# Kernel optimization log

Measured on AMD Instinct MI355X. Metric: run time of the kernel, lower is better.

## Reference

```python
import jax, jax.numpy as jnp
import numpy as np

D_MODEL = 1024
NUM_HEADS = 16
HEAD_DIM = D_MODEL // NUM_HEADS
B, TQ, TK = 4, 2048, 2048


def setup_inputs() -> dict:
    key = jax.random.key(0)
    ks = jax.random.split(key, 6)
    s = 1.0 / np.sqrt(D_MODEL)
    return {
        "x_q": jax.random.normal(ks[0], (B, TQ, D_MODEL), dtype=jnp.float32),
        "x_kv": jax.random.normal(ks[1], (B, TK, D_MODEL), dtype=jnp.float32),
        "attn_mask": jnp.zeros((TQ, TK), dtype=jnp.float32),
        "key_padding_mask": jnp.zeros((B, TK), dtype=bool),
        "Wq": jax.random.normal(ks[2], (D_MODEL, D_MODEL), dtype=jnp.float32) * s,
        "Wk": jax.random.normal(ks[3], (D_MODEL, D_MODEL), dtype=jnp.float32) * s,
        "Wv": jax.random.normal(ks[4], (D_MODEL, D_MODEL), dtype=jnp.float32) * s,
        "Wo": jax.random.normal(ks[5], (D_MODEL, D_MODEL), dtype=jnp.float32) * s,
    }


def reference(x_q, x_kv, attn_mask, key_padding_mask, Wq, Wk, Wv, Wo):
    b, tq, d = x_q.shape
    tk = x_kv.shape[1]
    h, hd = NUM_HEADS, HEAD_DIM
    # Linear(bias=False): y = x @ W.T ; split heads -> (b, h, t, hd)
    q = (x_q @ Wq.T).reshape(b, tq, h, hd).transpose(0, 2, 1, 3)
    k = (x_kv @ Wk.T).reshape(b, tk, h, hd).transpose(0, 2, 1, 3)
    v = (x_kv @ Wv.T).reshape(b, tk, h, hd).transpose(0, 2, 1, 3)
    scores = jnp.einsum("bhqd,bhkd->bhqk", q, k) / jnp.sqrt(jnp.float32(hd))
    scores = scores + attn_mask  # additive mask broadcasts over (b, h)
    scores = jnp.where(key_padding_mask[:, None, None, :], -jnp.inf, scores)
    w = jax.nn.softmax(scores, axis=-1)
    out = jnp.einsum("bhqk,bhkd->bhqd", w, v)  # (b, h, tq, hd)
    out = out.transpose(0, 2, 1, 3).reshape(b, tq, d)
    return out @ Wo.T
```

## Files before the change

### kernel.cpp

```cpp
#include <hip/hip_runtime.h>
#include <hip/hip_bf16.h>

#define TQ 2048
#define TKV 2048
#define NH 16
#define HD 64
#define DM 1024
#define BSZ 4
#define LOG2E 1.44269504088896340736f

typedef __bf16 bf16_t;
typedef bf16_t bf16x8 __attribute__((ext_vector_type(8)));
typedef bf16_t bf16x4 __attribute__((ext_vector_type(4)));
typedef float f32x4 __attribute__((ext_vector_type(4)));

__device__ __forceinline__ f32x4 MFMA16(bf16x8 a, bf16x8 b, f32x4 c) {
  return __builtin_amdgcn_mfma_f32_16x16x32_bf16(a, b, c, 0, 0, 0);
}

__device__ __forceinline__ void gload_lds16(const void* g, void* l) {
  __builtin_amdgcn_global_load_lds((const __attribute__((address_space(1))) void*)g,
                                   (__attribute__((address_space(3))) void*)l,
                                   16, 0, 0);
}

__device__ __forceinline__ int pl_idx(int q, int k) {
  int bb = (k >> 3) ^ (q & 7);
  return q * 64 + bb * 8 + (k & 7);
}

__device__ __forceinline__ int kv_idx(int row, int slot) {
  return row * 64 + (slot ^ (row & 7)) * 8;
}

__global__ __launch_bounds__(256) void cvt_all(
    const float* __restrict__ xq, const float* __restrict__ xkv,
    const float* __restrict__ wq, const float* __restrict__ wk,
    const float* __restrict__ wv, const float* __restrict__ wo,
    const unsigned char* __restrict__ kpad,
    bf16_t* __restrict__ oxq, bf16_t* __restrict__ oxkv,
    bf16_t* __restrict__ owq, bf16_t* __restrict__ owk,
    bf16_t* __restrict__ owv, bf16_t* __restrict__ owo,
    bf16_t* __restrict__ okpd) {
  const int blk = blockIdx.x;
  if (blk >= 10240) {
    const int i = (blk - 10240) * 256 + threadIdx.x;
    unsigned long long bits = *reinterpret_cast<const unsigned long long*>(kpad + (size_t)i * 8);
    bf16x8 o;
#pragma unroll
    for (int j = 0; j < 8; ++j)
      o[j] = ((bits >> (8 * j)) & 0xffull) ? (bf16_t)(-__builtin_inff()) : (bf16_t)0.f;
    reinterpret_cast<bf16x8*>(okpd)[i] = o;
    return;
  }
  const float* src;
  bf16_t* dst;
  int base;
  if (blk < 4096)      { src = xq;  dst = oxq;  base = blk; }
  else if (blk < 8192) { src = xkv; dst = oxkv; base = blk - 4096; }
  else if (blk < 8704) { src = wq;  dst = owq;  base = blk - 8192; }
  else if (blk < 9216) { src = wk;  dst = owk;  base = blk - 8704; }
  else if (blk < 9728) { src = wv;  dst = owv;  base = blk - 9216; }
  else                 { src = wo;  dst = owo;  base = blk - 9728; }
  const int i = base * 256 + threadIdx.x;
  const float4* p = reinterpret_cast<const float4*>(src) + 2 * (size_t)i;
  float4 a = p[0], b = p[1];
  bf16x8 o;
  o[0] = (bf16_t)a.x; o[1] = (bf16_t)a.y; o[2] = (bf16_t)a.z; o[3] = (bf16_t)a.w;
  o[4] = (bf16_t)b.x; o[5] = (bf16_t)b.y; o[6] = (bf16_t)b.z; o[7] = (bf16_t)b.w;
  reinterpret_cast<bf16x8*>(dst)[i] = o;
}

__global__ __launch_bounds__(256) void tmask(const float* __restrict__ am,
                                             bf16_t* __restrict__ amt) {
  __shared__ float T[64][65];
  const int q0 = blockIdx.x * 64, k0 = blockIdx.y * 64;
  const int tid = threadIdx.x;
  const int r = tid >> 2, c4 = (tid & 3) * 4;
#pragma unroll
  for (int cc = 0; cc < 4; ++cc) {
    const int kc = c4 + cc * 16;
    float4 v = *reinterpret_cast<const float4*>(am + (long)(q0 + r) * TKV + k0 + kc);
    T[kc + 0][r] = v.x; T[kc + 1][r] = v.y; T[kc + 2][r] = v.z; T[kc + 3][r] = v.w;
  }
  __syncthreads();
  const int kr = tid >> 2, qc0 = (tid & 3) * 16;
  bf16x8 o0, o1;
#pragma unroll
  for (int j = 0; j < 8; ++j) o0[j] = (bf16_t)(T[kr][qc0 + j] * LOG2E);
#pragma unroll
  for (int j = 0; j < 8; ++j) o1[j] = (bf16_t)(T[kr][qc0 + 8 + j] * LOG2E);
  *reinterpret_cast<bf16x8*>(amt + (long)(k0 + kr) * TQ + q0 + qc0) = o0;
  *reinterpret_cast<bf16x8*>(amt + (long)(k0 + kr) * TQ + q0 + qc0 + 8) = o1;
}

template <bool BF16_OUT>
__global__ __launch_bounds__(256) void gemm_bt(const bf16_t* __restrict__ A,
                                               const bf16_t* __restrict__ Bw,
                                               void* __restrict__ Cout,
                                               int M, int N, int K, float scale) {
  __shared__ __align__(16) bf16_t As[128 * 32];
  __shared__ __align__(16) bf16_t Bs[128 * 32];
  const int tid = threadIdx.x;
  const int l = tid & 63;
  const int w = tid >> 6;
  const int wr = w >> 1, wc = w & 1;
  const int l15 = l & 15, lg = l >> 4;
  const long bm = (long)blockIdx.x * 128;
  const long bn = (long)blockIdx.y * 128;

  f32x4 acc[4][4] = {};
  const int c0i = tid, c1i = 256 + tid;
  const long ar0 = (bm + (c0i >> 2)) * (long)K + (c0i & 3) * 8;
  const long ar1 = (bm + (c1i >> 2)) * (long)K + (c1i & 3) * 8;
  const long br0 = (bn + (c0i >> 2)) * (long)K + (c0i & 3) * 8;
  const long br1 = (bn + (c1i >> 2)) * (long)K + (c1i & 3) * 8;

  for (int k0 = 0; k0 < K; k0 += 32) {
    __syncthreads();
    gload_lds16(A + ar0 + k0, As + c0i * 8);
    gload_lds16(A + ar1 + k0, As + c1i * 8);
    gload_lds16(Bw + br0 + k0, Bs + c0i * 8);
    gload_lds16(Bw + br1 + k0, Bs + c1i * 8);
    __syncthreads();

    bf16x8 af[4], bfr[4];
#pragma unroll
    for (int i = 0; i < 4; ++i)
      af[i] = *reinterpret_cast<const bf16x8*>(As + (wr * 64 + i * 16 + l15) * 32 + lg * 8);
#pragma unroll
    for (int j = 0; j < 4; ++j)
      bfr[j] = *reinterpret_cast<const bf16x8*>(Bs + (wc * 64 + j * 16 + l15) * 32 + lg * 8);
#pragma unroll
    for (int i = 0; i < 4; ++i)
#pragma unroll
      for (int j = 0; j < 4; ++j)
        acc[i][j] = MFMA16(af[i], bfr[j], acc[i][j]);
  }

#pragma unroll
  for (int i = 0; i < 4; ++i)
#pragma unroll
    for (int j = 0; j < 4; ++j)
#pragma unroll
      for (int r = 0; r < 4; ++r) {
        long rg = bm + wr * 64 + i * 16 + lg * 4 + r;
        long cg = bn + wc * 64 + j * 16 + l15;
        float v = acc[i][j][r] * scale;
        if (BF16_OUT) ((bf16_t*)Cout)[rg * N + cg] = (bf16_t)v;
        else          ((float*)Cout)[rg * N + cg] = v;
      }
}

__global__ __launch_bounds__(256) void gemm_kv(const bf16_t* __restrict__ A,
                                               const bf16_t* __restrict__ Bw,
                                               bf16_t* __restrict__ Kb,
                                               bf16_t* __restrict__ VTb) {
  __shared__ __align__(16) bf16_t As[128 * 32];
  __shared__ __align__(16) bf16_t Bs[128 * 32];
  const int K = DM;
  const int tid = threadIdx.x;
  const int l = tid & 63;
  const int w = tid >> 6;
  const int wr = w >> 1, wc = w & 1;
  const int l15 = l & 15, lg = l >> 4;
  const long bm = (long)blockIdx.x * 128;
  const long bn = (long)blockIdx.y * 128;

  f32x4 acc[4][4] = {};
  const int c0i = tid, c1i = 256 + tid;
  const long ar0 = (bm + (c0i >> 2)) * (long)K + (c0i & 3) * 8;
  const long ar1 = (bm + (c1i >> 2)) * (long)K + (c1i & 3) * 8;
  const long br0 = (bn + (c0i >> 2)) * (long)K + (c0i & 3) * 8;
  const long br1 = (bn + (c1i >> 2)) * (long)K + (c1i & 3) * 8;

  for (int k0 = 0; k0 < K; k0 += 32) {
    __syncthreads();
    gload_lds16(A + ar0 + k0, As + c0i * 8);
    gload_lds16(A + ar1 + k0, As + c1i * 8);
    gload_lds16(Bw + br0 + k0, Bs + c0i * 8);
    gload_lds16(Bw + br1 + k0, Bs + c1i * 8);
    __syncthreads();

    bf16x8 af[4], bfr[4];
#pragma unroll
    for (int i = 0; i < 4; ++i)
      af[i] = *reinterpret_cast<const bf16x8*>(As + (wr * 64 + i * 16 + l15) * 32 + lg * 8);
#pragma unroll
    for (int j = 0; j < 4; ++j)
      bfr[j] = *reinterpret_cast<const bf16x8*>(Bs + (wc * 64 + j * 16 + l15) * 32 + lg * 8);
#pragma unroll
    for (int i = 0; i < 4; ++i)
#pragma unroll
      for (int j = 0; j < 4; ++j)
        acc[i][j] = MFMA16(af[i], bfr[j], acc[i][j]);
  }

  if (bn < 1024) {
#pragma unroll
    for (int i = 0; i < 4; ++i)
#pragma unroll
      for (int j = 0; j < 4; ++j)
#pragma unroll
        for (int r = 0; r < 4; ++r) {
          long rg = bm + wr * 64 + i * 16 + lg * 4 + r;
          long cg = bn + wc * 64 + j * 16 + l15;
          Kb[rg * DM + cg] = (bf16_t)acc[i][j][r];
        }
  } else {
    const long brow = (bm >> 11) * (long)DM;
    const long t0 = (bm & 2047);
#pragma unroll
    for (int i = 0; i < 4; ++i)
#pragma unroll
      for (int j = 0; j < 4; ++j) {
        long d = bn - 1024 + wc * 64 + j * 16 + l15;
        long t = t0 + wr * 64 + i * 16 + lg * 4;
        bf16x4 pk;
#pragma unroll
        for (int r = 0; r < 4; ++r) pk[r] = (bf16_t)acc[i][j][r];
        *reinterpret_cast<bf16x4*>(VTb + (brow + d) * TKV + t) = pk;
      }
  }
}

__global__ __launch_bounds__(256) void attn_fwd(const bf16_t* __restrict__ Qb,
                                                const bf16_t* __restrict__ Kb,
                                                const bf16_t* __restrict__ VTb,
                                                const bf16_t* __restrict__ amt,
                                                const bf16_t* __restrict__ kpd,
                                                bf16_t* __restrict__ Ob) {
  __shared__ __align__(16) bf16_t Ks[2][64 * 64];
  __shared__ __align__(16) bf16_t Vs[2][64 * 64];
  __shared__ __align__(16) bf16_t Pl[4][16 * 64];
  const int tid = threadIdx.x;
  const int w = tid >> 6, l = tid & 63;
  const int l15 = l & 15, lg = l >> 4;
  const int b = blockIdx.y >> 4, h = blockIdx.y & 15;
  const int q0 = blockIdx.x * 64 + w * 16;
  const long qbase = (long)b * TQ * DM;

  const bf16_t* qp = Qb + qbase + (long)(q0 + l15) * DM + h * HD + lg * 8;
  bf16x8 qf0 = *reinterpret_cast<const bf16x8*>(qp);
  bf16x8 qf1 = *reinterpret_cast<const bf16x8*>(qp + 32);

  const bf16_t* kg = Kb + qbase + h * HD;
  const bf16_t* vtg = VTb + ((long)b * DM + h * HD) * (long)TKV;

  const int srow0 = tid >> 3, spos0 = tid & 7;
  const int soff0 = (spos0 ^ (srow0 & 7)) * 8;
  const int srow1 = (tid + 256) >> 3, spos1 = tid & 7;
  const int soff1 = (spos1 ^ (srow1 & 7)) * 8;

  f32x4 o[4] = {};
  float m[4], ls[4];
#pragma unroll
  for (int r = 0; r < 4; ++r) { m[r] = -1e30f; ls[r] = 0.f; }

  gload_lds16(kg + (long)srow0 * DM + soff0, &Ks[0][tid * 8]);
  gload_lds16(kg + (long)srow1 * DM + soff1, &Ks[0][(tid + 256) * 8]);
  gload_lds16(vtg + (long)srow0 * TKV + soff0, &Vs[0][tid * 8]);
  gload_lds16(vtg + (long)srow1 * TKV + soff1, &Vs[0][(tid + 256) * 8]);
  __syncthreads();

  int cur = 0;
  const int NT = TKV / 64;
  for (int t = 0; t < NT; ++t) {
    const int k0 = t * 64;
    if (t + 1 < NT) {
      const long kn = (long)(k0 + 64);
      gload_lds16(kg + (kn + srow0) * DM + soff0, &Ks[cur ^ 1][tid * 8]);
      gload_lds16(kg + (kn + srow1) * DM + soff1, &Ks[cur ^ 1][(tid + 256) * 8]);
      gload_lds16(vtg + (long)srow0 * TKV + kn + soff0, &Vs[cur ^ 1][tid * 8]);
      gload_lds16(vtg + (long)srow1 * TKV + kn + soff1, &Vs[cur ^ 1][(tid + 256) * 8]);
    }
    const bf16_t* Kc = Ks[cur];
    const bf16_t* Vc = Vs[cur];

    bf16x4 mt[4];
    float kpf[4];
#pragma unroll
    for (int f = 0; f < 4; ++f) {
      mt[f] = *reinterpret_cast<const bf16x4*>(amt + (long)(k0 + 16 * f + l15) * TQ + q0 + lg * 4);
      kpf[f] = (float)kpd[b * TKV + k0 + 16 * f + l15];
    }

    f32x4 c[4] = {};
#pragma unroll
    for (int f = 0; f < 4; ++f) {
      const int row = 16 * f + l15;
      bf16x8 ka = *reinterpret_cast<const bf16x8*>(Kc + kv_idx(row, lg));
      bf16x8 kb = *reinterpret_cast<const bf16x8*>(Kc + kv_idx(row, 4 + lg));
      c[f] = MFMA16(qf0, ka, c[f]);
      c[f] = MFMA16(qf1, kb, c[f]);
    }

#pragma unroll
    for (int r = 0; r < 4; ++r) {
      float s0 = c[0][r] + (float)mt[0][r] + kpf[0];
      float s1 = c[1][r] + (float)mt[1][r] + kpf[1];
      float s2 = c[2][r] + (float)mt[2][r] + kpf[2];
      float s3 = c[3][r] + (float)mt[3][r] + kpf[3];
      float rmax = fmaxf(fmaxf(s0, s1), fmaxf(s2, s3));
#pragma unroll
      for (int d = 1; d < 16; d <<= 1) rmax = fmaxf(rmax, __shfl_xor(rmax, d, 64));
      const float mn = fmaxf(m[r], rmax);
      const float fac = exp2f(m[r] - mn);
      m[r] = mn;
      const float p0 = exp2f(s0 - mn);
      const float p1 = exp2f(s1 - mn);
      const float p2 = exp2f(s2 - mn);
      const float p3 = exp2f(s3 - mn);
      ls[r] = ls[r] * fac + (p0 + p1 + p2 + p3);
      o[0][r] *= fac; o[1][r] *= fac; o[2][r] *= fac; o[3][r] *= fac;
      const int q = lg * 4 + r;
      Pl[w][pl_idx(q, l15)]      = (bf16_t)p0;
      Pl[w][pl_idx(q, 16 + l15)] = (bf16_t)p1;
      Pl[w][pl_idx(q, 32 + l15)] = (bf16_t)p2;
      Pl[w][pl_idx(q, 48 + l15)] = (bf16_t)p3;
    }

#pragma unroll
    for (int hh = 0; hh < 2; ++hh) {
      bf16x8 pf = *reinterpret_cast<const bf16x8*>(&Pl[w][pl_idx(l15, hh * 32 + lg * 8)]);
#pragma unroll
      for (int f = 0; f < 4; ++f) {
        const int row = 16 * f + l15;
        bf16x8 vf = *reinterpret_cast<const bf16x8*>(Vc + kv_idx(row, hh * 4 + lg));
        o[f] = MFMA16(pf, vf, o[f]);
      }
    }

    __syncthreads();
    cur ^= 1;
  }

#pragma unroll
  for (int r = 0; r < 4; ++r) {
    float t = ls[r];
#pragma unroll
    for (int d = 1; d < 16; d <<= 1) t += __shfl_xor(t, d, 64);
    const float inv = t > 0.f ? 1.f / t : 0.f;
    const long qg = q0 + lg * 4 + r;
    bf16_t* op = Ob + qbase + qg * DM + h * HD;
    op[l15]      = (bf16_t)(o[0][r] * inv);
    op[16 + l15] = (bf16_t)(o[1][r] * inv);
    op[32 + l15] = (bf16_t)(o[2][r] * inv);
    op[48 + l15] = (bf16_t)(o[3][r] * inv);
  }
}

extern "C" void kernel_launch(void* const* d_in, const int* in_sizes, int n_in,
                              void* d_out, int out_size, void* d_ws, size_t ws_size,
                              hipStream_t stream) {
  const float* x_q = (const float*)d_in[0];
  const float* x_kv = (const float*)d_in[1];
  const float* amask = (const float*)d_in[2];
  const unsigned char* kpad = (const unsigned char*)d_in[3];
  const float* Wq = (const float*)d_in[4];
  const float* Wk = (const float*)d_in[5];
  const float* Wv = (const float*)d_in[6];
  const float* Wo = (const float*)d_in[7];
  float* out = (float*)d_out;

  char* ws = (char*)d_ws;
  const size_t MB = 1024ull * 1024ull;
  bf16_t* Ob    = (bf16_t*)(ws + 0 * MB);
  bf16_t* xq_b  = (bf16_t*)(ws + 0 * MB);
  bf16_t* xkv_b = (bf16_t*)(ws + 16 * MB);
  bf16_t* Qb    = (bf16_t*)(ws + 32 * MB);
  bf16_t* Kb    = (bf16_t*)(ws + 48 * MB);
  bf16_t* VTb   = (bf16_t*)(ws + 64 * MB);
  bf16_t* amt   = (bf16_t*)(ws + 80 * MB);
  bf16_t* Wq_b  = (bf16_t*)(ws + 88 * MB);
  bf16_t* Wk_b  = (bf16_t*)(ws + 90 * MB);
  bf16_t* Wv_b  = (bf16_t*)(ws + 92 * MB);
  bf16_t* Wo_b  = (bf16_t*)(ws + 94 * MB);
  bf16_t* kpdd  = (bf16_t*)(ws + 96 * MB);

  const int NTOK = BSZ * TQ;

  cvt_all<<<10244, 256, 0, stream>>>(x_q, x_kv, Wq, Wk, Wv, Wo, kpad,
                                     xq_b, xkv_b, Wq_b, Wk_b, Wv_b, Wo_b, kpdd);
  tmask<<<dim3(TQ / 64, TKV / 64), 256, 0, stream>>>(amask, amt);

  gemm_bt<true><<<dim3(NTOK / 128, DM / 128), 256, 0, stream>>>(
      xq_b, Wq_b, Qb, NTOK, DM, DM, 0.125f * LOG2E);
  gemm_kv<<<dim3(NTOK / 128, 2 * DM / 128), 256, 0, stream>>>(xkv_b, Wk_b, Kb, VTb);

  attn_fwd<<<dim3(TQ / 64, BSZ * NH), 256, 0, stream>>>(Qb, Kb, VTb, amt, kpdd, Ob);

  gemm_bt<false><<<dim3(NTOK / 128, DM / 128), 256, 0, stream>>>(
      Ob, Wo_b, out, NTOK, DM, DM, 1.f);
}
```

Baseline: 557.2 us.

## Fold padding mask into per-batch bias, double query rows per warp, lazy rescale

Attention blocks now handle 128 query rows, with each warp processing two 16-row groups. This reuses each K/V LDS fragment across two MFMA groups and halves K/V tile loads per query. The key padding mask is combined with the additive mask into a per-batch bf16 bias tensor, which preloads the score accumulator and removes the separate padding load. Online softmax now rescales only when the row max grows by more than 8 (log2 units). Blocks are also remapped for locality. The costs are a 4x larger mask tensor (32MB written and read), higher register pressure, and half as many blocks.

```diff
diff --git a/kernel.cpp b/kernel.cpp
--- a/kernel.cpp
+++ b/kernel.cpp
@@ -37,22 +37,10 @@
     const float* __restrict__ xq, const float* __restrict__ xkv,
     const float* __restrict__ wq, const float* __restrict__ wk,
     const float* __restrict__ wv, const float* __restrict__ wo,
-    const unsigned char* __restrict__ kpad,
     bf16_t* __restrict__ oxq, bf16_t* __restrict__ oxkv,
     bf16_t* __restrict__ owq, bf16_t* __restrict__ owk,
-    bf16_t* __restrict__ owv, bf16_t* __restrict__ owo,
-    bf16_t* __restrict__ okpd) {
+    bf16_t* __restrict__ owv, bf16_t* __restrict__ owo) {
   const int blk = blockIdx.x;
-  if (blk >= 10240) {
-    const int i = (blk - 10240) * 256 + threadIdx.x;
-    unsigned long long bits = *reinterpret_cast<const unsigned long long*>(kpad + (size_t)i * 8);
-    bf16x8 o;
-#pragma unroll
-    for (int j = 0; j < 8; ++j)
-      o[j] = ((bits >> (8 * j)) & 0xffull) ? (bf16_t)(-__builtin_inff()) : (bf16_t)0.f;
-    reinterpret_cast<bf16x8*>(okpd)[i] = o;
-    return;
-  }
   const float* src;
   bf16_t* dst;
   int base;
@@ -71,8 +59,9 @@
   reinterpret_cast<bf16x8*>(dst)[i] = o;
 }
 
-__global__ __launch_bounds__(256) void tmask(const float* __restrict__ am,
-                                             bf16_t* __restrict__ amt) {
+__global__ __launch_bounds__(256) void tmask2(const float* __restrict__ am,
+                                              const unsigned char* __restrict__ kpad,
+                                              bf16_t* __restrict__ amt2) {
   __shared__ float T[64][65];
   const int q0 = blockIdx.x * 64, k0 = blockIdx.y * 64;
   const int tid = threadIdx.x;
@@ -85,13 +74,21 @@
   }
   __syncthreads();
   const int kr = tid >> 2, qc0 = (tid & 3) * 16;
-  bf16x8 o0, o1;
-#pragma unroll
-  for (int j = 0; j < 8; ++j) o0[j] = (bf16_t)(T[kr][qc0 + j] * LOG2E);
-#pragma unroll
-  for (int j = 0; j < 8; ++j) o1[j] = (bf16_t)(T[kr][qc0 + 8 + j] * LOG2E);
-  *reinterpret_cast<bf16x8*>(amt + (long)(k0 + kr) * TQ + q0 + qc0) = o0;
-  *reinterpret_cast<bf16x8*>(amt + (long)(k0 + kr) * TQ + q0 + qc0 + 8) = o1;
+  float mk[16];
+#pragma unroll
+  for (int j = 0; j < 16; ++j) mk[j] = T[kr][qc0 + j] * LOG2E;
+#pragma unroll
+  for (int b = 0; b < BSZ; ++b) {
+    const float kv = kpad[b * TKV + k0 + kr] ? -__builtin_inff() : 0.f;
+    bf16x8 o0, o1;
+#pragma unroll
+    for (int j = 0; j < 8; ++j) o0[j] = (bf16_t)(mk[j] + kv);
+#pragma unroll
+    for (int j = 0; j < 8; ++j) o1[j] = (bf16_t)(mk[8 + j] + kv);
+    bf16_t* dst = amt2 + ((long)b * TKV + k0 + kr) * TQ + q0 + qc0;
+    *reinterpret_cast<bf16x8*>(dst) = o0;
+    *reinterpret_cast<bf16x8*>(dst + 8) = o1;
+  }
 }
 
 template <bool BF16_OUT>
@@ -227,8 +224,7 @@
 __global__ __launch_bounds__(256) void attn_fwd(const bf16_t* __restrict__ Qb,
                                                 const bf16_t* __restrict__ Kb,
                                                 const bf16_t* __restrict__ VTb,
-                                                const bf16_t* __restrict__ amt,
-                                                const bf16_t* __restrict__ kpd,
+                                                const bf16_t* __restrict__ amt2,
                                                 bf16_t* __restrict__ Ob) {
   __shared__ __align__(16) bf16_t Ks[2][64 * 64];
   __shared__ __align__(16) bf16_t Vs[2][64 * 64];
@@ -236,26 +232,36 @@
   const int tid = threadIdx.x;
   const int w = tid >> 6, l = tid & 63;
   const int l15 = l & 15, lg = l >> 4;
-  const int b = blockIdx.y >> 4, h = blockIdx.y & 15;
-  const int q0 = blockIdx.x * 64 + w * 16;
+
+  const int flat = blockIdx.y * 16 + blockIdx.x;
+  const int nid = (flat & 7) * 128 + (flat >> 3);
+  const int bh = nid >> 4, qb = nid & 15;
+  const int b = bh >> 4, h = bh & 15;
+  const int q0 = qb * 128 + w * 32;
   const long qbase = (long)b * TQ * DM;
 
   const bf16_t* qp = Qb + qbase + (long)(q0 + l15) * DM + h * HD + lg * 8;
-  bf16x8 qf0 = *reinterpret_cast<const bf16x8*>(qp);
-  bf16x8 qf1 = *reinterpret_cast<const bf16x8*>(qp + 32);
+  bf16x8 qf[2][2];
+  qf[0][0] = *reinterpret_cast<const bf16x8*>(qp);
+  qf[0][1] = *reinterpret_cast<const bf16x8*>(qp + 32);
+  qf[1][0] = *reinterpret_cast<const bf16x8*>(qp + 16 * DM);
+  qf[1][1] = *reinterpret_cast<const bf16x8*>(qp + 16 * DM + 32);
 
   const bf16_t* kg = Kb + qbase + h * HD;
   const bf16_t* vtg = VTb + ((long)b * DM + h * HD) * (long)TKV;
-
-  const int srow0 = tid >> 3, spos0 = tid & 7;
-  const int soff0 = (spos0 ^ (srow0 & 7)) * 8;
-  const int srow1 = (tid + 256) >> 3, spos1 = tid & 7;
-  const int soff1 = (spos1 ^ (srow1 & 7)) * 8;
-
-  f32x4 o[4] = {};
-  float m[4], ls[4];
-#pragma unroll
-  for (int r = 0; r < 4; ++r) { m[r] = -1e30f; ls[r] = 0.f; }
+  const bf16_t* m2 = amt2 + (long)b * TKV * TQ;
+
+  const int srow0 = tid >> 3;
+  const int soff0 = ((tid & 7) ^ (srow0 & 7)) * 8;
+  const int srow1 = (tid + 256) >> 3;
+  const int soff1 = ((tid & 7) ^ (srow1 & 7)) * 8;
+
+  f32x4 o[2][4] = {};
+  float m[2][4], ls[2][4];
+#pragma unroll
+  for (int g = 0; g < 2; ++g)
+#pragma unroll
+    for (int r = 0; r < 4; ++r) { m[g][r] = -1e30f; ls[g][r] = 0.f; }
 
   gload_lds16(kg + (long)srow0 * DM + soff0, &Ks[0][tid * 8]);
   gload_lds16(kg + (long)srow1 * DM + soff1, &Ks[0][(tid + 256) * 8]);
@@ -277,77 +283,92 @@
     const bf16_t* Kc = Ks[cur];
     const bf16_t* Vc = Vs[cur];
 
-    bf16x4 mt[4];
-    float kpf[4];
-#pragma unroll
-    for (int f = 0; f < 4; ++f) {
-      mt[f] = *reinterpret_cast<const bf16x4*>(amt + (long)(k0 + 16 * f + l15) * TQ + q0 + lg * 4);
-      kpf[f] = (float)kpd[b * TKV + k0 + 16 * f + l15];
-    }
-
-    f32x4 c[4] = {};
+    bf16x4 mt[2][4];
+#pragma unroll
+    for (int g = 0; g < 2; ++g)
+#pragma unroll
+      for (int f = 0; f < 4; ++f)
+        mt[g][f] = *reinterpret_cast<const bf16x4*>(
+            m2 + (long)(k0 + 16 * f + l15) * TQ + q0 + g * 16 + lg * 4);
+
+    f32x4 c[2][4];
+#pragma unroll
+    for (int g = 0; g < 2; ++g)
+#pragma unroll
+      for (int f = 0; f < 4; ++f)
+#pragma unroll
+        for (int r = 0; r < 4; ++r) c[g][f][r] = (float)mt[g][f][r];
+
 #pragma unroll
     for (int f = 0; f < 4; ++f) {
       const int row = 16 * f + l15;
       bf16x8 ka = *reinterpret_cast<const bf16x8*>(Kc + kv_idx(row, lg));
-      bf16x8 kb = *reinterpret_cast<const bf16x8*>(Kc + kv_idx(row, 4 + lg));
-      c[f] = MFMA16(qf0, ka, c[f]);
-      c[f] = MFMA16(qf1, kb, c[f]);
-    }
-
-#pragma unroll
-    for (int r = 0; r < 4; ++r) {
-      float s0 = c[0][r] + (float)mt[0][r] + kpf[0];
-      float s1 = c[1][r] + (float)mt[1][r] + kpf[1];
-      float s2 = c[2][r] + (float)mt[2][r] + kpf[2];
-      float s3 = c[3][r] + (float)mt[3][r] + kpf[3];
-      float rmax = fmaxf(fmaxf(s0, s1), fmaxf(s2, s3));
-#pragma unroll
-      for (int d = 1; d < 16; d <<= 1) rmax = fmaxf(rmax, __shfl_xor(rmax, d, 64));
-      const float mn = fmaxf(m[r], rmax);
-      const float fac = exp2f(m[r] - mn);
-      m[r] = mn;
-      const float p0 = exp2f(s0 - mn);
-      const float p1 = exp2f(s1 - mn);
-      const float p2 = exp2f(s2 - mn);
-      const float p3 = exp2f(s3 - mn);
-      ls[r] = ls[r] * fac + (p0 + p1 + p2 + p3);
-      o[0][r] *= fac; o[1][r] *= fac; o[2][r] *= fac; o[3][r] *= fac;
-      const int q = lg * 4 + r;
-      Pl[w][pl_idx(q, l15)]      = (bf16_t)p0;
-      Pl[w][pl_idx(q, 16 + l15)] = (bf16_t)p1;
-      Pl[w][pl_idx(q, 32 + l15)] = (bf16_t)p2;
-      Pl[w][pl_idx(q, 48 + l15)] = (bf16_t)p3;
-    }
-
-#pragma unroll
-    for (int hh = 0; hh < 2; ++hh) {
-      bf16x8 pf = *reinterpret_cast<const bf16x8*>(&Pl[w][pl_idx(l15, hh * 32 + lg * 8)]);
-#pragma unroll
-      for (int f = 0; f < 4; ++f) {
-        const int row = 16 * f + l15;
-        bf16x8 vf = *reinterpret_cast<const bf16x8*>(Vc + kv_idx(row, hh * 4 + lg));
-        o[f] = MFMA16(pf, vf, o[f]);
+      bf16x8 kb2 = *reinterpret_cast<const bf16x8*>(Kc + kv_idx(row, 4 + lg));
+#pragma unroll
+      for (int g = 0; g < 2; ++g) {
+        c[g][f] = MFMA16(qf[g][0], ka, c[g][f]);
+        c[g][f] = MFMA16(qf[g][1], kb2, c[g][f]);
       }
     }
 
+#pragma unroll
+    for (int g = 0; g < 2; ++g) {
+#pragma unroll
+      for (int r = 0; r < 4; ++r) {
+        const float s0 = c[g][0][r], s1 = c[g][1][r];
+        const float s2 = c[g][2][r], s3 = c[g][3][r];
+        float rmax = fmaxf(fmaxf(s0, s1), fmaxf(s2, s3));
+#pragma unroll
+        for (int d = 1; d < 16; d <<= 1) rmax = fmaxf(rmax, __shfl_xor(rmax, d, 64));
+        if (!__all(rmax <= m[g][r] + 8.f)) {
+          const float mn = fmaxf(m[g][r], rmax);
+          const float fac = exp2f(m[g][r] - mn);
+          ls[g][r] *= fac;
+          o[g][0][r] *= fac; o[g][1][r] *= fac;
+          o[g][2][r] *= fac; o[g][3][r] *= fac;
+          m[g][r] = mn;
+        }
+        const float p0 = exp2f(s0 - m[g][r]);
+        const float p1 = exp2f(s1 - m[g][r]);
+        const float p2 = exp2f(s2 - m[g][r]);
+        const float p3 = exp2f(s3 - m[g][r]);
+        ls[g][r] += (p0 + p1) + (p2 + p3);
+        const int q = lg * 4 + r;
+        Pl[w][pl_idx(q, l15)]      = (bf16_t)p0;
+        Pl[w][pl_idx(q, 16 + l15)] = (bf16_t)p1;
+        Pl[w][pl_idx(q, 32 + l15)] = (bf16_t)p2;
+        Pl[w][pl_idx(q, 48 + l15)] = (bf16_t)p3;
+      }
+#pragma unroll
+      for (int hh = 0; hh < 2; ++hh) {
+        bf16x8 pf = *reinterpret_cast<const bf16x8*>(&Pl[w][pl_idx(l15, hh * 32 + lg * 8)]);
+#pragma unroll
+        for (int f = 0; f < 4; ++f) {
+          bf16x8 vf = *reinterpret_cast<const bf16x8*>(Vc + kv_idx(16 * f + l15, hh * 4 + lg));
+          o[g][f] = MFMA16(pf, vf, o[g][f]);
+        }
+      }
+    }
+
     __syncthreads();
     cur ^= 1;
   }
 
 #pragma unroll
-  for (int r = 0; r < 4; ++r) {
-    float t = ls[r];
-#pragma unroll
-    for (int d = 1; d < 16; d <<= 1) t += __shfl_xor(t, d, 64);
-    const float inv = t > 0.f ? 1.f / t : 0.f;
-    const long qg = q0 + lg * 4 + r;
-    bf16_t* op = Ob + qbase + qg * DM + h * HD;
-    op[l15]      = (bf16_t)(o[0][r] * inv);
-    op[16 + l15] = (bf16_t)(o[1][r] * inv);
-    op[32 + l15] = (bf16_t)(o[2][r] * inv);
-    op[48 + l15] = (bf16_t)(o[3][r] * inv);
-  }
+  for (int g = 0; g < 2; ++g)
+#pragma unroll
+    for (int r = 0; r < 4; ++r) {
+      float t = ls[g][r];
+#pragma unroll
+      for (int d = 1; d < 16; d <<= 1) t += __shfl_xor(t, d, 64);
+      const float inv = t > 0.f ? 1.f / t : 0.f;
+      const long qg = q0 + g * 16 + lg * 4 + r;
+      bf16_t* op = Ob + qbase + qg * DM + h * HD;
+      op[l15]      = (bf16_t)(o[g][0][r] * inv);
+      op[16 + l15] = (bf16_t)(o[g][1][r] * inv);
+      op[32 + l15] = (bf16_t)(o[g][2][r] * inv);
+      op[48 + l15] = (bf16_t)(o[g][3][r] * inv);
+    }
 }
 
 extern "C" void kernel_launch(void* const* d_in, const int* in_sizes, int n_in,
@@ -365,30 +386,30 @@
 
   char* ws = (char*)d_ws;
   const size_t MB = 1024ull * 1024ull;
-  bf16_t* Ob    = (bf16_t*)(ws + 0 * MB);
   bf16_t* xq_b  = (bf16_t*)(ws + 0 * MB);
   bf16_t* xkv_b = (bf16_t*)(ws + 16 * MB);
+  bf16_t* amt2  = (bf16_t*)(ws + 0 * MB);
   bf16_t* Qb    = (bf16_t*)(ws + 32 * MB);
   bf16_t* Kb    = (bf16_t*)(ws + 48 * MB);
   bf16_t* VTb   = (bf16_t*)(ws + 64 * MB);
-  bf16_t* amt   = (bf16_t*)(ws + 80 * MB);
-  bf16_t* Wq_b  = (bf16_t*)(ws + 88 * MB);
-  bf16_t* Wk_b  = (bf16_t*)(ws + 90 * MB);
-  bf16_t* Wv_b  = (bf16_t*)(ws + 92 * MB);
-  bf16_t* Wo_b  = (bf16_t*)(ws + 94 * MB);
-  bf16_t* kpdd  = (bf16_t*)(ws + 96 * MB);
+  bf16_t* Ob    = (bf16_t*)(ws + 80 * MB);
+  bf16_t* Wq_b  = (bf16_t*)(ws + 96 * MB);
+  bf16_t* Wk_b  = (bf16_t*)(ws + 98 * MB);
+  bf16_t* Wv_b  = (bf16_t*)(ws + 100 * MB);
+  bf16_t* Wo_b  = (bf16_t*)(ws + 102 * MB);
 
   const int NTOK = BSZ * TQ;
 
-  cvt_all<<<10244, 256, 0, stream>>>(x_q, x_kv, Wq, Wk, Wv, Wo, kpad,
-                                     xq_b, xkv_b, Wq_b, Wk_b, Wv_b, Wo_b, kpdd);
-  tmask<<<dim3(TQ / 64, TKV / 64), 256, 0, stream>>>(amask, amt);
+  cvt_all<<<10240, 256, 0, stream>>>(x_q, x_kv, Wq, Wk, Wv, Wo,
+                                     xq_b, xkv_b, Wq_b, Wk_b, Wv_b, Wo_b);
 
   gemm_bt<true><<<dim3(NTOK / 128, DM / 128), 256, 0, stream>>>(
       xq_b, Wq_b, Qb, NTOK, DM, DM, 0.125f * LOG2E);
   gemm_kv<<<dim3(NTOK / 128, 2 * DM / 128), 256, 0, stream>>>(xkv_b, Wk_b, Kb, VTb);
 
-  attn_fwd<<<dim3(TQ / 64, BSZ * NH), 256, 0, stream>>>(Qb, Kb, VTb, amt, kpdd, Ob);
+  tmask2<<<dim3(TQ / 64, TKV / 64), 256, 0, stream>>>(amask, kpad, amt2);
+
+  attn_fwd<<<dim3(16, 64), 256, 0, stream>>>(Qb, Kb, VTb, amt2, Ob);
 
   gemm_bt<false><<<dim3(NTOK / 128, DM / 128), 256, 0, stream>>>(
       Ob, Wo_b, out, NTOK, DM, DM, 1.f);
```

Measured after the change: 516.6 us. -7.3%, faster.
